# Performance work log

Measured on AMD Instinct MI355X. Metric: run time of the kernel, lower is better.

The kernel has to match this reference:

```python
import jax, jax.numpy as jnp
import numpy as np

B, M, D = 2048, 128, 5          # batch, max_atoms, max_degree
F_A, F_B, C = 62, 6, 128        # atom feats, bond feats, conv_width


def setup_inputs() -> dict:
    key = jax.random.key(0)
    k1, k2, k3, k4, k5 = jax.random.split(key, 5)
    atoms = jax.random.normal(k1, (B, M, F_A), dtype=jnp.float32)
    bonds = jax.random.uniform(k2, (B, M, D, F_B), dtype=jnp.float32)
    # edges in [-1, M-1]; -1 = no neighbour (padding)
    edges = jax.random.randint(k3, (B, M, D), 0, M + 1, dtype=jnp.int32) - 1
    fan = F_A + F_B
    scale = float(np.sqrt(2.0 / (fan + C)))
    W_inner = jax.random.normal(k4, (D, fan, C), dtype=jnp.float32) * scale
    b_inner = jnp.zeros((D, C), dtype=jnp.float32)
    W_self = jax.random.normal(k5, (fan, C), dtype=jnp.float32) * scale
    b_self = jnp.zeros((C,), dtype=jnp.float32)
    return {"atoms": atoms, "bonds": bonds, "edges": edges,
            "W_inner": W_inner, "b_inner": b_inner,
            "W_self": W_self, "b_self": b_self}


def reference(atoms, bonds, edges, W_inner, b_inner, W_self, b_self):
    # --- encode() of TiedGraphAutoencoder (encode_only=True) ---
    b = atoms.shape[0]
    # atom degree = number of non-(-1) entries per atom  (B, M)
    deg = jnp.sum((edges != -1).astype(jnp.float32), axis=-1)

    # neighbour_lookup: pad a zero atom at index 0, shift edges by +1,
    # batched gather -> (B, M, D, F_A)
    padded = jnp.pad(atoms, ((0, 0), (1, 0), (0, 0)))
    neigh = padded[jnp.arange(b)[:, None, None], edges + 1]

    summed_atoms = neigh.sum(axis=-2)          # (B, M, F_A)
    summed_bonds = bonds.sum(axis=-2)          # (B, M, F_B)
    summed_features = jnp.concatenate([summed_atoms, summed_bonds], axis=-1)

    # per-degree TimeDistributed Dense + relu, masked by (deg == d), summed
    h = jax.nn.relu(jnp.einsum('bmf,dfc->bmdc', summed_features, W_inner)
                    + b_inner)                 # (B, M, D, C)
    mask = (deg[..., None] == jnp.arange(D, dtype=jnp.float32)).astype(h.dtype)
    zni = jnp.einsum('bmdc,bmd->bmc', h, mask)  # (B, M, C)

    # self connection: dense on [atoms, summed_bonds]
    vxi = jnp.concatenate([atoms, summed_bonds], axis=-1)
    zxi = jax.nn.relu(vxi @ W_self + b_self)    # (B, M, C)

    return zni + zxi
```

## Files before the change

kernel.cpp:

```cpp
#include <hip/hip_runtime.h>

#define NB 2048
#define NM 128
#define ND 5
#define NFA 62
#define NFB 6
#define NFAN 68
#define NC 128
#define KP 96

typedef __bf16 bf16x8 __attribute__((ext_vector_type(8)));
typedef float floatx4 __attribute__((ext_vector_type(4)));

__device__ __forceinline__ unsigned short f2bf(float x) {
    unsigned u = __builtin_bit_cast(unsigned, x);
    u += 0x7FFFu + ((u >> 16) & 1u);
    return (unsigned short)(u >> 16);
}

__global__ __launch_bounds__(256) void prep_w(const float* __restrict__ W_self,
                                              unsigned short* __restrict__ wsb) {
    const int i = blockIdx.x * 256 + threadIdx.x;
    const int c = i / KP;
    const int f = i - c * KP;
    unsigned short v = 0;
    if (f < NFAN) v = f2bf(W_self[f * NC + c]);
    wsb[i] = v;
}

__device__ __forceinline__ bf16x8 load8(const float* p) {
    float2 v0 = *(const float2*)(p);
    float2 v1 = *(const float2*)(p + 2);
    float2 v2 = *(const float2*)(p + 4);
    float2 v3 = *(const float2*)(p + 6);
    bf16x8 r;
    r[0] = (__bf16)v0.x; r[1] = (__bf16)v0.y; r[2] = (__bf16)v1.x; r[3] = (__bf16)v1.y;
    r[4] = (__bf16)v2.x; r[5] = (__bf16)v2.y; r[6] = (__bf16)v3.x; r[7] = (__bf16)v3.y;
    return r;
}

__device__ __forceinline__ bf16x8 load6bs(const float* p, const float* bs) {
    float2 v0 = *(const float2*)(p);
    float2 v1 = *(const float2*)(p + 2);
    float2 v2 = *(const float2*)(p + 4);
    float2 b01 = *(const float2*)(bs);
    bf16x8 r;
    r[0] = (__bf16)v0.x; r[1] = (__bf16)v0.y; r[2] = (__bf16)v1.x; r[3] = (__bf16)v1.y;
    r[4] = (__bf16)v2.x; r[5] = (__bf16)v2.y; r[6] = (__bf16)b01.x; r[7] = (__bf16)b01.y;
    return r;
}

__global__ __launch_bounds__(256) void tga_wave(
    const float* __restrict__ atoms,
    const float* __restrict__ bonds,
    const int*   __restrict__ edges,
    const float* __restrict__ W_inner,
    const float* __restrict__ b_inner,
    const float* __restrict__ b_self,
    const unsigned short* __restrict__ wsb,
    float* __restrict__ out)
{
    __shared__ __align__(16) float s_bsf[4][32][8];
    __shared__ float s_sf[4][64];

    const int tid  = threadIdx.x;
    const int w    = tid >> 6;
    const int lane = tid & 63;
    const int b    = blockIdx.x;
    const int m0   = w * 32;

    const float* atoms_b = atoms + (size_t)b * (NM * NFA);
    const float* bonds_b = bonds + (size_t)b * (NM * ND * NFB);
    const int*   edges_b = edges + (size_t)b * (NM * ND);
    float*       out_b   = out   + (size_t)b * (NM * NC);

    int E0 = -1, E1 = -1, E2 = -1, E3 = -1, E4 = -1, deg = ND;
    if (lane < 32) {
        const int* e = edges_b + (m0 + lane) * ND;
        E0 = e[0]; E1 = e[1]; E2 = e[2]; E3 = e[3]; E4 = e[4];
        deg = (E0 >= 0) + (E1 >= 0) + (E2 >= 0) + (E3 >= 0) + (E4 >= 0);
    }
    unsigned long long smask = __ballot((lane < 32) && (deg < ND));

    {
        const int rb = lane >> 1, half = lane & 1;
        const float* bp = bonds_b + (m0 + rb) * (ND * NFB);
        float sb[NFB] = {0.f, 0.f, 0.f, 0.f, 0.f, 0.f};
        if (half == 0) {
            #pragma unroll
            for (int p = 0; p < 8; ++p) {
                float2 v = *(const float2*)&bp[2 * p];
                sb[(2 * p) % NFB]     += v.x;
                sb[(2 * p + 1) % NFB] += v.y;
            }
        } else {
            #pragma unroll
            for (int p = 8; p < 15; ++p) {
                float2 v = *(const float2*)&bp[2 * p];
                sb[(2 * p) % NFB]     += v.x;
                sb[(2 * p + 1) % NFB] += v.y;
            }
        }
        #pragma unroll
        for (int j = 0; j < NFB; ++j) sb[j] += __shfl_xor(sb[j], 1);
        if (half == 0) {
            *(float4*)&s_bsf[w][rb][0] = make_float4(sb[2], sb[3], sb[4], sb[5]);
            *(float2*)&s_bsf[w][rb][4] = make_float2(sb[0], sb[1]);
        }
    }
    __builtin_amdgcn_wave_barrier();

    const int col = lane & 15, quad = lane >> 4;
    const int lr0 = col, lr1 = 16 + col;
    const float* p0 = atoms_b + (m0 + lr0) * NFA;
    const float* p1 = atoms_b + (m0 + lr1) * NFA;

    bf16x8 a00 = load8(p0 + quad * 8);
    bf16x8 a10 = load8(p1 + quad * 8);
    bf16x8 a01, a11;
    if (quad < 3) {
        a01 = load8(p0 + 32 + quad * 8);
        a11 = load8(p1 + 32 + quad * 8);
    } else {
        a01 = load6bs(p0 + 56, &s_bsf[w][lr0][4]);
        a11 = load6bs(p1 + 56, &s_bsf[w][lr1][4]);
    }
    bf16x8 a02, a12;
    #pragma unroll
    for (int j = 0; j < 8; ++j) { a02[j] = (__bf16)0.f; a12[j] = (__bf16)0.f; }
    if (quad == 0) {
        float4 q0 = *(const float4*)&s_bsf[w][lr0][0];
        float4 q1 = *(const float4*)&s_bsf[w][lr1][0];
        a02[0] = (__bf16)q0.x; a02[1] = (__bf16)q0.y; a02[2] = (__bf16)q0.z; a02[3] = (__bf16)q0.w;
        a12[0] = (__bf16)q1.x; a12[1] = (__bf16)q1.y; a12[2] = (__bf16)q1.z; a12[3] = (__bf16)q1.w;
    }

    floatx4 acc[16];
    #pragma unroll
    for (int t = 0; t < 16; ++t) { floatx4 z; z[0] = z[1] = z[2] = z[3] = 0.f; acc[t] = z; }

    const unsigned short* wbase = wsb + (size_t)col * KP + quad * 8;
    #pragma unroll
    for (int ct = 0; ct < 8; ++ct) {
        bf16x8 wf0 = *(const bf16x8*)(wbase + ct * 16 * KP);
        bf16x8 wf1 = *(const bf16x8*)(wbase + ct * 16 * KP + 32);
        bf16x8 wf2 = *(const bf16x8*)(wbase + ct * 16 * KP + 64);
        acc[ct]     = __builtin_amdgcn_mfma_f32_16x16x32_bf16(a00, wf0, acc[ct],     0, 0, 0);
        acc[8 + ct] = __builtin_amdgcn_mfma_f32_16x16x32_bf16(a10, wf0, acc[8 + ct], 0, 0, 0);
        acc[ct]     = __builtin_amdgcn_mfma_f32_16x16x32_bf16(a01, wf1, acc[ct],     0, 0, 0);
        acc[8 + ct] = __builtin_amdgcn_mfma_f32_16x16x32_bf16(a11, wf1, acc[8 + ct], 0, 0, 0);
        acc[ct]     = __builtin_amdgcn_mfma_f32_16x16x32_bf16(a02, wf2, acc[ct],     0, 0, 0);
        acc[8 + ct] = __builtin_amdgcn_mfma_f32_16x16x32_bf16(a12, wf2, acc[8 + ct], 0, 0, 0);
    }

    #pragma unroll
    for (int ct = 0; ct < 8; ++ct) {
        const float bias = b_self[ct * 16 + col];
        #pragma unroll
        for (int rr = 0; rr < 4; ++rr) {
            const int row0 = m0 + quad * 4 + rr;
            out_b[row0 * NC + ct * 16 + col]        = fmaxf(acc[ct][rr]     + bias, 0.f);
            out_b[(row0 + 16) * NC + ct * 16 + col] = fmaxf(acc[8 + ct][rr] + bias, 0.f);
        }
    }

    while (smask) {
        const int ml = __ffsll(smask) - 1;
        smask &= smask - 1;
        const int m  = m0 + ml;
        const int d  = __shfl(deg, ml);
        const int e0 = __shfl(E0, ml), e1 = __shfl(E1, ml), e2 = __shfl(E2, ml),
                  e3 = __shfl(E3, ml), e4 = __shfl(E4, ml);

        if (lane < NFA) {
            float sv = 0.f;
            if (e0 >= 0) sv += atoms_b[e0 * NFA + lane];
            if (e1 >= 0) sv += atoms_b[e1 * NFA + lane];
            if (e2 >= 0) sv += atoms_b[e2 * NFA + lane];
            if (e3 >= 0) sv += atoms_b[e3 * NFA + lane];
            if (e4 >= 0) sv += atoms_b[e4 * NFA + lane];
            s_sf[w][lane] = sv;
        }
        __builtin_amdgcn_wave_barrier();

        const int c0 = 2 * lane;
        float2 bi = *(const float2*)&b_inner[d * NC + c0];
        float acc0 = bi.x, acc1 = bi.y;
        const float* Wd = W_inner + (size_t)d * (NFAN * NC);
        #pragma unroll
        for (int f = 0; f < NFA; ++f) {
            const float sfv = s_sf[w][f];
            float2 wv = *(const float2*)&Wd[f * NC + c0];
            acc0 += sfv * wv.x; acc1 += sfv * wv.y;
        }
        {
            const float* bb = &s_bsf[w][ml][0];
            const float fv[6] = {bb[4], bb[5], bb[0], bb[1], bb[2], bb[3]};
            #pragma unroll
            for (int j = 0; j < NFB; ++j) {
                float2 wv = *(const float2*)&Wd[(NFA + j) * NC + c0];
                acc0 += fv[j] * wv.x; acc1 += fv[j] * wv.y;
            }
        }
        float2 cur = *(float2*)&out_b[m * NC + c0];
        cur.x += fmaxf(acc0, 0.f);
        cur.y += fmaxf(acc1, 0.f);
        *(float2*)&out_b[m * NC + c0] = cur;
        __builtin_amdgcn_wave_barrier();
    }
}

extern "C" void kernel_launch(void* const* d_in, const int* in_sizes, int n_in,
                              void* d_out, int out_size, void* d_ws, size_t ws_size,
                              hipStream_t stream) {
    const float* atoms   = (const float*)d_in[0];
    const float* bonds   = (const float*)d_in[1];
    const int*   edges   = (const int*)d_in[2];
    const float* W_inner = (const float*)d_in[3];
    const float* b_inner = (const float*)d_in[4];
    const float* W_self  = (const float*)d_in[5];
    const float* b_self  = (const float*)d_in[6];
    float* out = (float*)d_out;
    unsigned short* wsb = (unsigned short*)d_ws;

    prep_w<<<(NC * KP + 255) / 256, 256, 0, stream>>>(W_self, wsb);
    tga_wave<<<NB, 256, 0, stream>>>(atoms, bonds, edges, W_inner, b_inner,
                                     b_self, wsb, out);
}
```

Measured before the change: 264.2 us.

## Stage bf16 W_self and per-batch atoms tile into LDS via global_load_lds

Each block now copies the padded bf16 W_self matrix and its full 128x62 atoms tile into shared memory with asynchronous global-to-LDS loads, then does the MFMA A/B fragment loads and the neighbour gathers from LDS instead of global memory. The W row stride drops from 96 to 88 elements, which shrinks the copy and changes the LDS bank mapping. The wave-local barrier becomes a block-wide __syncthreads so the LDS data is visible to all waves. This raises LDS use to roughly 59 KB per block, which can lower occupancy, and the copy depends on the memory wait completing before the barrier.

```diff
diff --git a/kernel.cpp b/kernel.cpp
--- a/kernel.cpp
+++ b/kernel.cpp
@@ -7,7 +7,7 @@
 #define NFB 6
 #define NFAN 68
 #define NC 128
-#define KP 96
+#define KP 88
 
 typedef __bf16 bf16x8 __attribute__((ext_vector_type(8)));
 typedef float floatx4 __attribute__((ext_vector_type(4)));
@@ -26,6 +26,13 @@
     unsigned short v = 0;
     if (f < NFAN) v = f2bf(W_self[f * NC + c]);
     wsb[i] = v;
+}
+
+__device__ __forceinline__ void glds16(const void* g, void* l) {
+    __builtin_amdgcn_global_load_lds(
+        (const __attribute__((address_space(1))) unsigned int*)g,
+        (__attribute__((address_space(3))) unsigned int*)l,
+        16, 0, 0);
 }
 
 __device__ __forceinline__ bf16x8 load8(const float* p) {
@@ -60,6 +67,8 @@
     const unsigned short* __restrict__ wsb,
     float* __restrict__ out)
 {
+    __shared__ __align__(16) unsigned short s_w[NC * KP + 8];
+    __shared__ __align__(16) float s_atoms[NM * NFA];
     __shared__ __align__(16) float s_bsf[4][32][8];
     __shared__ float s_sf[4][64];
 
@@ -73,6 +82,17 @@
     const float* bonds_b = bonds + (size_t)b * (NM * ND * NFB);
     const int*   edges_b = edges + (size_t)b * (NM * ND);
     float*       out_b   = out   + (size_t)b * (NM * NC);
+
+    {
+        const char* gw = (const char*)wsb;
+        const char* ga = (const char*)atoms_b;
+        char* lw = (char*)s_w;
+        char* la = (char*)s_atoms;
+        for (int ch = w; ch < 22; ch += 4)
+            glds16(gw + ch * 1024 + lane * 16, lw + ch * 1024);
+        for (int ch = w; ch < 31; ch += 4)
+            glds16(ga + ch * 1024 + lane * 16, la + ch * 1024);
+    }
 
     int E0 = -1, E1 = -1, E2 = -1, E3 = -1, E4 = -1, deg = ND;
     if (lane < 32) {
@@ -108,12 +128,13 @@
             *(float2*)&s_bsf[w][rb][4] = make_float2(sb[0], sb[1]);
         }
     }
-    __builtin_amdgcn_wave_barrier();
+
+    __syncthreads();
 
     const int col = lane & 15, quad = lane >> 4;
     const int lr0 = col, lr1 = 16 + col;
-    const float* p0 = atoms_b + (m0 + lr0) * NFA;
-    const float* p1 = atoms_b + (m0 + lr1) * NFA;
+    const float* p0 = s_atoms + (m0 + lr0) * NFA;
+    const float* p1 = s_atoms + (m0 + lr1) * NFA;
 
     bf16x8 a00 = load8(p0 + quad * 8);
     bf16x8 a10 = load8(p1 + quad * 8);
@@ -139,12 +160,13 @@
     #pragma unroll
     for (int t = 0; t < 16; ++t) { floatx4 z; z[0] = z[1] = z[2] = z[3] = 0.f; acc[t] = z; }
 
-    const unsigned short* wbase = wsb + (size_t)col * KP + quad * 8;
+    const unsigned short* wbase = s_w + col * KP + quad * 8;
     #pragma unroll
     for (int ct = 0; ct < 8; ++ct) {
-        bf16x8 wf0 = *(const bf16x8*)(wbase + ct * 16 * KP);
-        bf16x8 wf1 = *(const bf16x8*)(wbase + ct * 16 * KP + 32);
-        bf16x8 wf2 = *(const bf16x8*)(wbase + ct * 16 * KP + 64);
+        const unsigned short* wc = wbase + ct * 16 * KP;
+        bf16x8 wf0 = *(const bf16x8*)(wc);
+        bf16x8 wf1 = *(const bf16x8*)(wc + 32);
+        bf16x8 wf2 = *(const bf16x8*)(wc + 64);
         acc[ct]     = __builtin_amdgcn_mfma_f32_16x16x32_bf16(a00, wf0, acc[ct],     0, 0, 0);
         acc[8 + ct] = __builtin_amdgcn_mfma_f32_16x16x32_bf16(a10, wf0, acc[8 + ct], 0, 0, 0);
         acc[ct]     = __builtin_amdgcn_mfma_f32_16x16x32_bf16(a01, wf1, acc[ct],     0, 0, 0);
@@ -174,11 +196,11 @@
 
         if (lane < NFA) {
             float sv = 0.f;
-            if (e0 >= 0) sv += atoms_b[e0 * NFA + lane];
-            if (e1 >= 0) sv += atoms_b[e1 * NFA + lane];
-            if (e2 >= 0) sv += atoms_b[e2 * NFA + lane];
-            if (e3 >= 0) sv += atoms_b[e3 * NFA + lane];
-            if (e4 >= 0) sv += atoms_b[e4 * NFA + lane];
+            if (e0 >= 0) sv += s_atoms[e0 * NFA + lane];
+            if (e1 >= 0) sv += s_atoms[e1 * NFA + lane];
+            if (e2 >= 0) sv += s_atoms[e2 * NFA + lane];
+            if (e3 >= 0) sv += s_atoms[e3 * NFA + lane];
+            if (e4 >= 0) sv += s_atoms[e4 * NFA + lane];
             s_sf[w][lane] = sv;
         }
         __builtin_amdgcn_wave_barrier();
@@ -223,7 +245,7 @@
     float* out = (float*)d_out;
     unsigned short* wsb = (unsigned short*)d_ws;
 
-    prep_w<<<(NC * KP + 255) / 256, 256, 0, stream>>>(W_self, wsb);
+    prep_w<<<(NC * KP) / 256, 256, 0, stream>>>(W_self, wsb);
     tga_wave<<<NB, 256, 0, stream>>>(atoms, bonds, edges, W_inner, b_inner,
                                      b_self, wsb, out);
 }
```

After: 247.4 us. -6.3%, faster.

## Stage W_self bf16 fragments in LDS via direct global-to-LDS loads

Applied to the files above, without the earlier changes.

The prep kernel now writes W_self in MFMA-fragment order, so each lane's 8-element B operand is contiguous per (column tile, K slice). Each block copies the 24 KB pre-swizzled weight into shared memory with global_load_lds and reads MFMA operands from LDS instead of strided global loads. This targets redundant per-wave global traffic for the weights. In exchange it adds a block-wide __syncthreads and 24 KB of LDS per block, which may lower occupancy.

```diff
diff --git a/kernel.cpp b/kernel.cpp
--- a/kernel.cpp
+++ b/kernel.cpp
@@ -7,7 +7,7 @@
 #define NFB 6
 #define NFAN 68
 #define NC 128
-#define KP 96
+#define KTOT 96
 
 typedef __bf16 bf16x8 __attribute__((ext_vector_type(8)));
 typedef float floatx4 __attribute__((ext_vector_type(4)));
@@ -21,11 +21,26 @@
 __global__ __launch_bounds__(256) void prep_w(const float* __restrict__ W_self,
                                               unsigned short* __restrict__ wsb) {
     const int i = blockIdx.x * 256 + threadIdx.x;
-    const int c = i / KP;
-    const int f = i - c * KP;
+    const int e     = i & 7;
+    const int chunk = i >> 3;
+    const int lane  = chunk & 63;
+    const int cs    = chunk >> 6;
+    const int ct    = cs / 3;
+    const int slice = cs - 3 * ct;
+    const int quad  = lane >> 4;
+    const int col   = lane & 15;
+    const int k     = slice * 32 + quad * 8 + e;
+    const int c     = ct * 16 + col;
     unsigned short v = 0;
-    if (f < NFAN) v = f2bf(W_self[f * NC + c]);
+    if (k < NFAN) v = f2bf(W_self[k * NC + c]);
     wsb[i] = v;
+}
+
+__device__ __forceinline__ void glds16(const void* g, void* l) {
+    __builtin_amdgcn_global_load_lds(
+        (const __attribute__((address_space(1))) unsigned int*)g,
+        (__attribute__((address_space(3))) unsigned int*)l,
+        16, 0, 0);
 }
 
 __device__ __forceinline__ bf16x8 load8(const float* p) {
@@ -60,6 +75,7 @@
     const unsigned short* __restrict__ wsb,
     float* __restrict__ out)
 {
+    __shared__ __align__(16) unsigned short s_w[NC * KTOT];
     __shared__ __align__(16) float s_bsf[4][32][8];
     __shared__ float s_sf[4][64];
 
@@ -73,6 +89,13 @@
     const float* bonds_b = bonds + (size_t)b * (NM * ND * NFB);
     const int*   edges_b = edges + (size_t)b * (NM * ND);
     float*       out_b   = out   + (size_t)b * (NM * NC);
+
+    {
+        const char* gw = (const char*)wsb;
+        char* lw = (char*)s_w;
+        for (int ch = w; ch < 24; ch += 4)
+            glds16(gw + ch * 1024 + lane * 16, lw + ch * 1024);
+    }
 
     int E0 = -1, E1 = -1, E2 = -1, E3 = -1, E4 = -1, deg = ND;
     if (lane < 32) {
@@ -108,7 +131,6 @@
             *(float2*)&s_bsf[w][rb][4] = make_float2(sb[0], sb[1]);
         }
     }
-    __builtin_amdgcn_wave_barrier();
 
     const int col = lane & 15, quad = lane >> 4;
     const int lr0 = col, lr1 = 16 + col;
@@ -117,6 +139,9 @@
 
     bf16x8 a00 = load8(p0 + quad * 8);
     bf16x8 a10 = load8(p1 + quad * 8);
+
+    __syncthreads();
+
     bf16x8 a01, a11;
     if (quad < 3) {
         a01 = load8(p0 + 32 + quad * 8);
@@ -139,12 +164,12 @@
     #pragma unroll
     for (int t = 0; t < 16; ++t) { floatx4 z; z[0] = z[1] = z[2] = z[3] = 0.f; acc[t] = z; }
 
-    const unsigned short* wbase = wsb + (size_t)col * KP + quad * 8;
+    const unsigned short* wl = s_w + lane * 8;
     #pragma unroll
     for (int ct = 0; ct < 8; ++ct) {
-        bf16x8 wf0 = *(const bf16x8*)(wbase + ct * 16 * KP);
-        bf16x8 wf1 = *(const bf16x8*)(wbase + ct * 16 * KP + 32);
-        bf16x8 wf2 = *(const bf16x8*)(wbase + ct * 16 * KP + 64);
+        bf16x8 wf0 = *(const bf16x8*)(wl + (ct * 3 + 0) * 512);
+        bf16x8 wf1 = *(const bf16x8*)(wl + (ct * 3 + 1) * 512);
+        bf16x8 wf2 = *(const bf16x8*)(wl + (ct * 3 + 2) * 512);
         acc[ct]     = __builtin_amdgcn_mfma_f32_16x16x32_bf16(a00, wf0, acc[ct],     0, 0, 0);
         acc[8 + ct] = __builtin_amdgcn_mfma_f32_16x16x32_bf16(a10, wf0, acc[8 + ct], 0, 0, 0);
         acc[ct]     = __builtin_amdgcn_mfma_f32_16x16x32_bf16(a01, wf1, acc[ct],     0, 0, 0);
@@ -223,7 +248,7 @@
     float* out = (float*)d_out;
     unsigned short* wsb = (unsigned short*)d_ws;
 
-    prep_w<<<(NC * KP + 255) / 256, 256, 0, stream>>>(W_self, wsb);
+    prep_w<<<(NC * KTOT) / 256, 256, 0, stream>>>(W_self, wsb);
     tga_wave<<<NB, 256, 0, stream>>>(atoms, bonds, edges, W_inner, b_inner,
                                      b_self, wsb, out);
 }
```

Result: faster. 257.3 us (-2.6%).
